# Kernel optimization log

Hardware: AMD Instinct MI355X
Metric: run time of the kernel (lower is better)

Reference implementation:

```python
import jax, jax.numpy as jnp
import numpy as np

EPS = 1e-5
GROUPS = 16
OUT_CH = 128
GC = OUT_CH // GROUPS  # group_channels = 8
SPAN = 128


def _bn(x, gamma, beta, axes):
    # BatchNorm in training mode: biased batch statistics over `axes`.
    m = jnp.mean(x, axis=axes, keepdims=True)
    v = jnp.var(x, axis=axes, keepdims=True)
    shape = [1] * x.ndim
    shape[1] = x.shape[1]
    g = gamma.reshape(shape)
    b = beta.reshape(shape)
    return (x - m) * jax.lax.rsqrt(v + EPS) * g + b


def setup_inputs() -> dict:
    key = jax.random.key(0)
    ks = jax.random.split(key, 3)
    x = jax.random.normal(ks[0], (2, 128, 64, 128), dtype=jnp.float32)
    W_qkv = jax.random.normal(ks[1], (2 * OUT_CH, 128), dtype=jnp.float32) * (1.0 / np.sqrt(128))
    rel_emb = jax.random.normal(ks[2], (2 * GC, 2 * SPAN - 1), dtype=jnp.float32)
    return {
        "x": x,
        "W_qkv": W_qkv,
        "gamma_qkv": jnp.ones((2 * OUT_CH,), jnp.float32),
        "beta_qkv": jnp.zeros((2 * OUT_CH,), jnp.float32),
        "rel_emb": rel_emb,
        "gamma_sim": jnp.ones((3 * GROUPS,), jnp.float32),
        "beta_sim": jnp.zeros((3 * GROUPS,), jnp.float32),
        "gamma_out": jnp.ones((2 * OUT_CH,), jnp.float32),
        "beta_out": jnp.zeros((2 * OUT_CH,), jnp.float32),
    }


def reference(x, W_qkv, gamma_qkv, beta_qkv, rel_emb, gamma_sim, beta_sim, gamma_out, beta_out):
    # dim == 1: attend over the width axis. x: [B, C, H, W], W == SPAN.
    B, C, H, W = x.shape
    xr = jnp.transpose(x, (0, 2, 1, 3)).reshape(B * H, C, W)  # [BH, C, W]

    # 1x1 Conv1d + BN1d -> query/key/value
    qkv = jnp.einsum('oc,bcl->bol', W_qkv, xr)  # [BH, 2*OUT, W]
    qkv = _bn(qkv, gamma_qkv, beta_qkv, axes=(0, 2))
    qkv = qkv.reshape(B * H, GROUPS, 2 * GC, W)
    q = qkv[:, :, : GC // 2]            # [BH, g, gc/2, W]
    k = qkv[:, :, GC // 2: GC]          # [BH, g, gc/2, W]
    v = qkv[:, :, GC:]                  # [BH, g, gc,   W]

    # relative position embeddings gathered into [2*gc, span, span]
    idx = jnp.arange(SPAN)[:, None] - jnp.arange(SPAN)[None, :] + SPAN - 1
    emb = rel_emb[:, idx]               # [2*gc, span, span]
    q_emb = emb[: GC // 2]
    k_emb = emb[GC // 2: GC]
    v_emb = emb[GC:]

    qe = jnp.einsum('bgci,cij->bgij', q, q_emb)   # [BH, g, W, W]
    ke = jnp.einsum('bgci,cij->bgij', k, k_emb)   # [BH, g, W, W]
    # faithful to original: contracts the first spatial axis of qe/ke
    qk = jnp.einsum('bgci,bgcj->bgij', qe, ke)    # [BH, g, W, W]

    sim = jnp.concatenate([qk, qe, ke], axis=1)   # [BH, 3g, W, W]
    sim = _bn(sim, gamma_sim, beta_sim, axes=(0, 2, 3))
    sim = sim.reshape(B * H, 3, GROUPS, W, W).sum(axis=1)  # [BH, g, W, W]
    sim = jax.nn.softmax(sim, axis=3)

    am = jnp.einsum('bgij,bgcj->bgci', sim, v)      # [BH, g, gc, W]
    ame = jnp.einsum('bgij,cij->bgci', sim, v_emb)  # [BH, g, gc, W]

    out = jnp.concatenate([am, ame], axis=-1).reshape(B * H, 2 * OUT_CH, W)
    out = _bn(out, gamma_out, beta_out, axes=(0, 2))
    out = out.reshape(B, H, OUT_CH, 2, W).sum(axis=-2)  # [B, H, OUT, W]
    return jnp.transpose(out, (0, 2, 1, 3))             # [B, OUT, H, W]
```

## Files before the change

kernel.cpp:

```cpp
#include <hip/hip_runtime.h>

#define EPS 1e-5f
typedef unsigned short u16;
typedef unsigned int u32;

typedef __attribute__((ext_vector_type(8))) short bf16x8;
typedef __attribute__((ext_vector_type(4))) float f32x4;

__device__ __forceinline__ float bf2f(u16 h) {
    u32 u = ((u32)h) << 16;
    return __builtin_bit_cast(float, u);
}
__device__ __forceinline__ u16 f2bf(float f) {
    u32 u = __builtin_bit_cast(u32, f);
    u32 r = (u + 0x7fffu + ((u >> 16) & 1u)) >> 16;
    return (u16)r;
}
__device__ __forceinline__ u32 pack2(float a, float b) {
    return (u32)f2bf(a) | ((u32)f2bf(b) << 16);
}

__global__ __launch_bounds__(256) void k1_gemm_qkv(
    const float* __restrict__ x, const float* __restrict__ Wq,
    float* __restrict__ qkv, float* __restrict__ stats)
{
    __shared__ float Wt[64 * 68];
    __shared__ float xt[64 * 128];
    const int tid = threadIdx.x;
    const int ot = blockIdx.x;
    const int n  = blockIdx.y;
    const int b = n >> 6, h = n & 63;
    const int to = tid >> 5, tl = tid & 31;
    const int o0 = to * 8, l0 = tl * 4;

    float acc[8][4];
#pragma unroll
    for (int r = 0; r < 8; ++r) { acc[r][0]=0.f; acc[r][1]=0.f; acc[r][2]=0.f; acc[r][3]=0.f; }

    for (int cb = 0; cb < 128; cb += 64) {
        __syncthreads();
#pragma unroll
        for (int k = 0; k < 4; ++k) {
            int f = tid + k * 256;
            int oo = f >> 4, c4 = f & 15;
            float4 v = *(const float4*)(Wq + (ot * 64 + oo) * 128 + cb + c4 * 4);
            *(float4*)(Wt + oo * 68 + c4 * 4) = v;
        }
#pragma unroll
        for (int k = 0; k < 8; ++k) {
            int f = tid + k * 256;
            int c = f >> 5, l4 = f & 31;
            float4 v = *(const float4*)(x + ((size_t)((b * 128 + cb + c) * 64 + h)) * 128 + l4 * 4);
            *(float4*)(xt + c * 128 + l4 * 4) = v;
        }
        __syncthreads();
#pragma unroll 4
        for (int c = 0; c < 64; ++c) {
            float4 xv = *(const float4*)(xt + c * 128 + l0);
#pragma unroll
            for (int r = 0; r < 8; ++r) {
                float w = Wt[(o0 + r) * 68 + c];
                acc[r][0] += w * xv.x; acc[r][1] += w * xv.y;
                acc[r][2] += w * xv.z; acc[r][3] += w * xv.w;
            }
        }
    }

#pragma unroll
    for (int r = 0; r < 8; ++r) {
        int o = ot * 64 + o0 + r;
        *(float4*)(qkv + ((size_t)n * 256 + o) * 128 + l0) =
            make_float4(acc[r][0], acc[r][1], acc[r][2], acc[r][3]);
        float s  = acc[r][0] + acc[r][1] + acc[r][2] + acc[r][3];
        float sq = acc[r][0]*acc[r][0] + acc[r][1]*acc[r][1] + acc[r][2]*acc[r][2] + acc[r][3]*acc[r][3];
#pragma unroll
        for (int m = 1; m < 32; m <<= 1) {
            s  += __shfl_xor(s, m);
            sq += __shfl_xor(sq, m);
        }
        if (tl == 0) {
            atomicAdd(&stats[o], s);
            atomicAdd(&stats[256 + o], sq);
        }
    }
}

__global__ void k3_coef_qkv(const float* __restrict__ stats,
                            const float* __restrict__ gamma, const float* __restrict__ beta,
                            float* __restrict__ coef)
{
    int o = threadIdx.x;
    const float cnt = 16384.f;
    float mean = stats[o] / cnt;
    float var  = stats[256 + o] / cnt - mean * mean;
    float a = gamma[o] * rsqrtf(var + EPS);
    coef[o] = a;
    coef[256 + o] = beta[o] - a * mean;
}

__global__ __launch_bounds__(512, 4) void k4_pass1(
    const float* __restrict__ qkv, const float* __restrict__ rel,
    const float* __restrict__ cq, u16* __restrict__ qk,
    float* __restrict__ stats)
{
    __shared__ u16 QEb[128 * 136];
    __shared__ u16 KEb[128 * 136];
    __shared__ float red[8 * 6];
    const int tid = threadIdx.x;
    const int n = blockIdx.x >> 4, g = blockIdx.x & 15;

    const int pt = tid & 31, pi = tid >> 5;
    const int t0 = pt * 4, i0 = pi * 8;
    const int d0 = t0 - i0 + 120;

    float qes = 0.f, qesq = 0.f, kes = 0.f, kesq = 0.f;

#pragma unroll
    for (int mat = 0; mat < 2; ++mat) {
        float qv[4][4];
#pragma unroll
        for (int c = 0; c < 4; ++c) {
            int o = g * 16 + mat * 4 + c;
            float a = cq[o], bb = cq[256 + o];
            float4 x0 = *(const float4*)(qkv + ((size_t)n * 256 + o) * 128 + t0);
            qv[c][0] = fmaf(a, x0.x, bb); qv[c][1] = fmaf(a, x0.y, bb);
            qv[c][2] = fmaf(a, x0.z, bb); qv[c][3] = fmaf(a, x0.w, bb);
        }
        float rr[4][12];
#pragma unroll
        for (int c = 0; c < 4; ++c) {
            const float* p = rel + (mat * 4 + c) * 255 + d0;
#pragma unroll
            for (int j = 0; j < 3; ++j) {
                float4 v = *(const float4*)(p + j * 4);
                rr[c][j*4+0] = v.x; rr[c][j*4+1] = v.y;
                rr[c][j*4+2] = v.z; rr[c][j*4+3] = v.w;
            }
        }
        u16* MB = mat ? KEb : QEb;
        float s = 0.f, sq = 0.f;
#pragma unroll
        for (int ii = 0; ii < 8; ++ii) {
            float vv[4];
#pragma unroll
            for (int tt = 0; tt < 4; ++tt) {
                int dl = tt - ii + 7;
                float v = qv[0][tt] * rr[0][dl] + qv[1][tt] * rr[1][dl]
                        + qv[2][tt] * rr[2][dl] + qv[3][tt] * rr[3][dl];
                vv[tt] = v;
                s += v; sq = fmaf(v, v, sq);
            }
            *(uint2*)(MB + (i0 + ii) * 136 + t0) =
                make_uint2(pack2(vv[0], vv[1]), pack2(vv[2], vv[3]));
        }
        if (mat == 0) { qes = s; qesq = sq; } else { kes = s; kesq = sq; }
    }
    __syncthreads();

    const int lane = tid & 63, wv = tid >> 6;
    const int fm = lane & 15, fq = lane >> 4;

    f32x4 acc[8];
#pragma unroll
    for (int tj = 0; tj < 8; ++tj) acc[tj] = (f32x4){0.f, 0.f, 0.f, 0.f};

#pragma unroll
    for (int kb = 0; kb < 4; ++kb) {
        const int ko = kb * 32 + fq * 8;
        bf16x8 a0 = *(const bf16x8*)(QEb + (wv * 16 + fm) * 136 + ko);
#pragma unroll
        for (int tj = 0; tj < 8; ++tj) {
            bf16x8 bfr = *(const bf16x8*)(KEb + (tj * 16 + fm) * 136 + ko);
            acc[tj] = __builtin_amdgcn_mfma_f32_16x16x32_bf16(a0, bfr, acc[tj], 0, 0, 0);
        }
    }

    float qks = 0.f, qksq = 0.f;
#pragma unroll
    for (int tj = 0; tj < 8; ++tj) {
#pragma unroll
        for (int r = 0; r < 4; ++r) {
            float v = acc[tj][r];
            qks += v; qksq = fmaf(v, v, qksq);
            QEb[(wv * 16 + fq * 4 + r) * 136 + tj * 16 + fm] = f2bf(v);
        }
    }

#pragma unroll
    for (int m = 1; m < 64; m <<= 1) {
        qes += __shfl_xor(qes, m);  qesq += __shfl_xor(qesq, m);
        kes += __shfl_xor(kes, m);  kesq += __shfl_xor(kesq, m);
        qks += __shfl_xor(qks, m);  qksq += __shfl_xor(qksq, m);
    }
    if (lane == 0) {
        red[wv * 6 + 0] = qes; red[wv * 6 + 1] = qesq;
        red[wv * 6 + 2] = kes; red[wv * 6 + 3] = kesq;
        red[wv * 6 + 4] = qks; red[wv * 6 + 5] = qksq;
    }
    __syncthreads();

    u16* qkg = qk + (size_t)(n * 16 + g) * 16384;
#pragma unroll
    for (int k = 0; k < 4; ++k) {
        int f = tid + k * 512;
        int row = f >> 4, c8 = f & 15;
        uint4 v = *(const uint4*)(QEb + row * 136 + c8 * 8);
        *(uint4*)(qkg + row * 128 + c8 * 8) = v;
    }

    if (tid < 6) {
        float tot = 0.f;
#pragma unroll
        for (int w = 0; w < 8; ++w) tot += red[w * 6 + tid];
        int off = (tid & 1) ? 560 : 512;
        int ch = (tid < 2) ? (16 + g) : (tid < 4) ? (32 + g) : g;
        atomicAdd(&stats[off + ch], tot);
    }
}

__global__ void k5_coef_sim(const float* __restrict__ stats,
                            const float* __restrict__ gamma, const float* __restrict__ beta,
                            float* __restrict__ coef)
{
    int ch = threadIdx.x;
    if (ch < 48) {
        const float cnt = 2097152.f;
        float mean = stats[512 + ch] / cnt;
        float var  = stats[560 + ch] / cnt - mean * mean;
        float a = gamma[ch] * rsqrtf(var + EPS);
        coef[ch] = a;
        coef[48 + ch] = beta[ch] - a * mean;
    }
}

__global__ __launch_bounds__(256, 4) void k6_pass2(
    const float* __restrict__ qkv, const float* __restrict__ rel,
    const float* __restrict__ cq, const float* __restrict__ cs,
    const u16* __restrict__ qk,
    float* __restrict__ outraw, float* __restrict__ ostats)
{
    __shared__ float relT[255 * 20];
    __shared__ float qv_s[2048];
    __shared__ float ot_s[16 * 132];
    const int tid = threadIdx.x;
    const int n = blockIdx.x >> 4, g = blockIdx.x & 15;

#pragma unroll
    for (int k = 0; k < 16; ++k) {
        int f = tid + k * 256;
        int d = f >> 4, c = f & 15;
        if (d < 255) relT[d * 20 + c] = rel[c * 255 + d];
    }
#pragma unroll
    for (int k = 0; k < 8; ++k) {
        int f = tid + k * 256;
        int row = f >> 7, t = f & 127;
        int o = g * 16 + row;
        qv_s[f] = cq[o] * qkv[((size_t)n * 256 + o) * 128 + t] + cq[256 + o];
    }
    __syncthreads();

    const float aqk = cs[g], aqe = cs[16 + g], ake = cs[32 + g];
    const float bsum = cs[48 + g] + cs[64 + g] + cs[80 + g];
    const int lane = tid & 63, wv = tid >> 6;
    const int r = lane >> 4, q = lane & 15;

    float vreg[8][8];
#pragma unroll
    for (int jj = 0; jj < 8; ++jj) {
        int j = q + 16 * jj;
#pragma unroll
        for (int c = 0; c < 8; ++c) vreg[jj][c] = qv_s[1024 + c * 128 + j];
    }
    const u16* qkg = qk + (size_t)(n * 16 + g) * 16384;

    for (int it = 0; it < 8; ++it) {
        int i = wv * 32 + it * 4 + r;
        float q0 = qv_s[i], q1 = qv_s[128 + i], q2 = qv_s[256 + i], q3 = qv_s[384 + i];
        float k0 = qv_s[512 + i], k1 = qv_s[640 + i], k2 = qv_s[768 + i], k3 = qv_s[896 + i];
        const u16* qkrow = qkg + i * 128;
        float s[8]; float mx = -3.0e38f;
#pragma unroll
        for (int jj = 0; jj < 8; ++jj) {
            int j = q + 16 * jj;
            int d = i - j + 127;
            float4 rq = *(const float4*)(relT + d * 20);
            float4 rk = *(const float4*)(relT + d * 20 + 4);
            float qe = q0 * rq.x + q1 * rq.y + q2 * rq.z + q3 * rq.w;
            float ke = k0 * rk.x + k1 * rk.y + k2 * rk.z + k3 * rk.w;
            float qkf = bf2f(qkrow[j]);
            float sv = aqk * qkf + aqe * qe + ake * ke + bsum;
            s[jj] = sv; mx = fmaxf(mx, sv);
        }
#pragma unroll
        for (int m = 1; m < 16; m <<= 1) mx = fmaxf(mx, __shfl_xor(mx, m));
        float es = 0.f; float e[8];
#pragma unroll
        for (int jj = 0; jj < 8; ++jj) { e[jj] = __expf(s[jj] - mx); es += e[jj]; }
#pragma unroll
        for (int m = 1; m < 16; m <<= 1) es += __shfl_xor(es, m);

        float am[8], ame[8];
#pragma unroll
        for (int c = 0; c < 8; ++c) { am[c] = 0.f; ame[c] = 0.f; }
#pragma unroll
        for (int jj = 0; jj < 8; ++jj) {
            int d = i - (q + 16 * jj) + 127;
            float4 r0 = *(const float4*)(relT + d * 20 + 8);
            float4 r1 = *(const float4*)(relT + d * 20 + 12);
            float ej = e[jj];
#pragma unroll
            for (int c = 0; c < 8; ++c) am[c] += ej * vreg[jj][c];
            ame[0] += ej * r0.x; ame[1] += ej * r0.y; ame[2] += ej * r0.z; ame[3] += ej * r0.w;
            ame[4] += ej * r1.x; ame[5] += ej * r1.y; ame[6] += ej * r1.z; ame[7] += ej * r1.w;
        }
#pragma unroll
        for (int m = 1; m < 16; m <<= 1) {
#pragma unroll
            for (int c = 0; c < 8; ++c) {
                am[c]  += __shfl_xor(am[c], m);
                ame[c] += __shfl_xor(ame[c], m);
            }
        }
        float inv = 1.f / es;
        float sel = 0.f;
#pragma unroll
        for (int c = 0; c < 8; ++c) {
            sel = (q == c)     ? am[c]  : sel;
            sel = (q == c + 8) ? ame[c] : sel;
        }
        int ch16 = (q < 8) ? (2 * q) : (2 * (q - 8) + 1);
        ot_s[ch16 * 132 + i] = sel * inv;
    }
    __syncthreads();

#pragma unroll
    for (int k = 0; k < 8; ++k) {
        int f = tid + k * 256;
        int ch16 = f >> 7, i = f & 127;
        float v = ot_s[ch16 * 132 + i];
        outraw[((size_t)n * 256 + g * 16 + ch16) * 128 + i] = v;
        float sv = v, sq = v * v;
#pragma unroll
        for (int m = 1; m < 64; m <<= 1) { sv += __shfl_xor(sv, m); sq += __shfl_xor(sq, m); }
        if (lane == 0) {
            atomicAdd(&ostats[g * 16 + ch16], sv);
            atomicAdd(&ostats[256 + g * 16 + ch16], sq);
        }
    }
}

__global__ void k7_coef_out(const float* __restrict__ stats,
                            const float* __restrict__ gamma, const float* __restrict__ beta,
                            float* __restrict__ coef)
{
    int o = threadIdx.x;
    const float cnt = 16384.f;
    float mean = stats[608 + o] / cnt;
    float var  = stats[864 + o] / cnt - mean * mean;
    float a = gamma[o] * rsqrtf(var + EPS);
    coef[o] = a;
    coef[256 + o] = beta[o] - a * mean;
}

__global__ __launch_bounds__(256) void k8_final(
    const float* __restrict__ outraw, const float* __restrict__ co,
    float* __restrict__ out)
{
    int idx = blockIdx.x * 256 + threadIdx.x;
    int w  = idx & 127;
    int h  = (idx >> 7) & 63;
    int oc = (idx >> 13) & 127;
    int b  = idx >> 20;
    int n  = b * 64 + h;
    int o0 = oc * 2;
    float x0 = outraw[((size_t)n * 256 + o0) * 128 + w];
    float x1 = outraw[((size_t)n * 256 + o0 + 1) * 128 + w];
    out[idx] = (co[o0] * x0 + co[256 + o0]) + (co[o0 + 1] * x1 + co[256 + o0 + 1]);
}

extern "C" void kernel_launch(void* const* d_in, const int* in_sizes, int n_in,
                              void* d_out, int out_size, void* d_ws, size_t ws_size,
                              hipStream_t stream)
{
    const float* x   = (const float*)d_in[0];
    const float* Wq  = (const float*)d_in[1];
    const float* gq  = (const float*)d_in[2];
    const float* bq  = (const float*)d_in[3];
    const float* rel = (const float*)d_in[4];
    const float* gs  = (const float*)d_in[5];
    const float* bs  = (const float*)d_in[6];
    const float* go  = (const float*)d_in[7];
    const float* bo  = (const float*)d_in[8];

    float* ws     = (float*)d_ws;
    float* qkv    = ws;
    float* outraw = ws + 4194304;
    u16*   qk     = (u16*)(ws + 8388608);
    float* stats  = ws + 25165824;
    float* cq     = stats + 1120;
    float* cs     = stats + 1632;
    float* co     = stats + 1728;

    (void)hipMemsetAsync(stats, 0, 1120 * sizeof(float), stream);

    k1_gemm_qkv<<<dim3(4, 128), 256, 0, stream>>>(x, Wq, qkv, stats);
    k3_coef_qkv<<<1, 256, 0, stream>>>(stats, gq, bq, cq);
    k4_pass1<<<2048, 512, 0, stream>>>(qkv, rel, cq, qk, stats);
    k5_coef_sim<<<1, 64, 0, stream>>>(stats, gs, bs, cs);
    k6_pass2<<<2048, 256, 0, stream>>>(qkv, rel, cq, cs, qk, outraw, stats + 608);
    k7_coef_out<<<1, 256, 0, stream>>>(stats, go, bo, co);
    k8_final<<<8192, 256, 0, stream>>>(outraw, co, (float*)d_out);
}
```

Measured before the change: 361.5 us.

## Rewrite attention pass as one-thread-per-row online softmax with bf16 LDS tables

```diff
diff --git a/kernel.cpp b/kernel.cpp
--- a/kernel.cpp
+++ b/kernel.cpp
@@ -233,119 +233,113 @@
     }
 }
 
-__global__ __launch_bounds__(256, 4) void k6_pass2(
+__global__ __launch_bounds__(128, 4) void k6_pass2(
     const float* __restrict__ qkv, const float* __restrict__ rel,
     const float* __restrict__ cq, const float* __restrict__ cs,
     const u16* __restrict__ qk,
     float* __restrict__ outraw, float* __restrict__ ostats)
 {
-    __shared__ float relT[255 * 20];
-    __shared__ float qv_s[2048];
-    __shared__ float ot_s[16 * 132];
+    __shared__ u16 relb[256 * 24];
+    __shared__ u16 vb[128 * 8];
+    __shared__ float qn_s[8 * 128];
     const int tid = threadIdx.x;
     const int n = blockIdx.x >> 4, g = blockIdx.x & 15;
 
 #pragma unroll
-    for (int k = 0; k < 16; ++k) {
-        int f = tid + k * 256;
-        int d = f >> 4, c = f & 15;
-        if (d < 255) relT[d * 20 + c] = rel[c * 255 + d];
+    for (int k = 0; k < 32; ++k) {
+        int f = tid + k * 128;
+        int c = f >> 8, d = f & 255;
+        if (d < 255) relb[d * 24 + c] = f2bf(rel[c * 255 + d]);
     }
 #pragma unroll
     for (int k = 0; k < 8; ++k) {
-        int f = tid + k * 256;
-        int row = f >> 7, t = f & 127;
-        int o = g * 16 + row;
-        qv_s[f] = cq[o] * qkv[((size_t)n * 256 + o) * 128 + t] + cq[256 + o];
+        int f = tid + k * 128;
+        int c = f >> 7, t = f & 127;
+        int o = g * 16 + c;
+        qn_s[f] = fmaf(cq[o], qkv[((size_t)n * 256 + o) * 128 + t], cq[256 + o]);
+    }
+#pragma unroll
+    for (int k = 0; k < 8; ++k) {
+        int f = tid + k * 128;
+        int c = f >> 7, j = f & 127;
+        int o = g * 16 + 8 + c;
+        float v = fmaf(cq[o], qkv[((size_t)n * 256 + o) * 128 + j], cq[256 + o]);
+        vb[j * 8 + c] = f2bf(v);
     }
     __syncthreads();
 
     const float aqk = cs[g], aqe = cs[16 + g], ake = cs[32 + g];
     const float bsum = cs[48 + g] + cs[64 + g] + cs[80 + g];
-    const int lane = tid & 63, wv = tid >> 6;
-    const int r = lane >> 4, q = lane & 15;
-
-    float vreg[8][8];
-#pragma unroll
-    for (int jj = 0; jj < 8; ++jj) {
-        int j = q + 16 * jj;
-#pragma unroll
-        for (int c = 0; c < 8; ++c) vreg[jj][c] = qv_s[1024 + c * 128 + j];
-    }
-    const u16* qkg = qk + (size_t)(n * 16 + g) * 16384;
-
-    for (int it = 0; it < 8; ++it) {
-        int i = wv * 32 + it * 4 + r;
-        float q0 = qv_s[i], q1 = qv_s[128 + i], q2 = qv_s[256 + i], q3 = qv_s[384 + i];
-        float k0 = qv_s[512 + i], k1 = qv_s[640 + i], k2 = qv_s[768 + i], k3 = qv_s[896 + i];
-        const u16* qkrow = qkg + i * 128;
-        float s[8]; float mx = -3.0e38f;
-#pragma unroll
-        for (int jj = 0; jj < 8; ++jj) {
-            int j = q + 16 * jj;
-            int d = i - j + 127;
-            float4 rq = *(const float4*)(relT + d * 20);
-            float4 rk = *(const float4*)(relT + d * 20 + 4);
-            float qe = q0 * rq.x + q1 * rq.y + q2 * rq.z + q3 * rq.w;
-            float ke = k0 * rk.x + k1 * rk.y + k2 * rk.z + k3 * rk.w;
-            float qkf = bf2f(qkrow[j]);
-            float sv = aqk * qkf + aqe * qe + ake * ke + bsum;
-            s[jj] = sv; mx = fmaxf(mx, sv);
-        }
-#pragma unroll
-        for (int m = 1; m < 16; m <<= 1) mx = fmaxf(mx, __shfl_xor(mx, m));
-        float es = 0.f; float e[8];
-#pragma unroll
-        for (int jj = 0; jj < 8; ++jj) { e[jj] = __expf(s[jj] - mx); es += e[jj]; }
-#pragma unroll
-        for (int m = 1; m < 16; m <<= 1) es += __shfl_xor(es, m);
-
-        float am[8], ame[8];
-#pragma unroll
-        for (int c = 0; c < 8; ++c) { am[c] = 0.f; ame[c] = 0.f; }
-#pragma unroll
-        for (int jj = 0; jj < 8; ++jj) {
-            int d = i - (q + 16 * jj) + 127;
-            float4 r0 = *(const float4*)(relT + d * 20 + 8);
-            float4 r1 = *(const float4*)(relT + d * 20 + 12);
-            float ej = e[jj];
-#pragma unroll
-            for (int c = 0; c < 8; ++c) am[c] += ej * vreg[jj][c];
-            ame[0] += ej * r0.x; ame[1] += ej * r0.y; ame[2] += ej * r0.z; ame[3] += ej * r0.w;
-            ame[4] += ej * r1.x; ame[5] += ej * r1.y; ame[6] += ej * r1.z; ame[7] += ej * r1.w;
-        }
-#pragma unroll
-        for (int m = 1; m < 16; m <<= 1) {
+    const int i = tid;
+
+    float q0 = qn_s[i],       q1 = qn_s[128 + i], q2 = qn_s[256 + i], q3 = qn_s[384 + i];
+    float k0 = qn_s[512 + i], k1 = qn_s[640 + i], k2 = qn_s[768 + i], k3 = qn_s[896 + i];
+
+    const u16* qkrow = qk + (size_t)(n * 16 + g) * 16384 + i * 128;
+
+    float m = -3.0e38f, l = 0.f;
+    float am[8], ame[8];
+#pragma unroll
+    for (int c = 0; c < 8; ++c) { am[c] = 0.f; ame[c] = 0.f; }
+
+#pragma unroll
+    for (int jc = 0; jc < 8; ++jc) {
+        union { uint4 v[2]; u16 h[16]; } qh;
+        qh.v[0] = *(const uint4*)(qkrow + jc * 16);
+        qh.v[1] = *(const uint4*)(qkrow + jc * 16 + 8);
+
+        const int dbase = i + 127 - jc * 16;
+        float s[16]; float mc = -3.0e38f;
+#pragma unroll
+        for (int jl = 0; jl < 16; ++jl) {
+            int d = dbase - jl;
+            bf16x8 rb = *(const bf16x8*)(relb + d * 24);
+            float qe = q0 * bf2f((u16)rb[0]) + q1 * bf2f((u16)rb[1])
+                     + q2 * bf2f((u16)rb[2]) + q3 * bf2f((u16)rb[3]);
+            float ke = k0 * bf2f((u16)rb[4]) + k1 * bf2f((u16)rb[5])
+                     + k2 * bf2f((u16)rb[6]) + k3 * bf2f((u16)rb[7]);
+            float sv = aqk * bf2f(qh.h[jl]) + aqe * qe + ake * ke + bsum;
+            s[jl] = sv; mc = fmaxf(mc, sv);
+        }
+        float mn = fmaxf(m, mc);
+        float sc = __expf(m - mn);
+        l *= sc;
+#pragma unroll
+        for (int c = 0; c < 8; ++c) { am[c] *= sc; ame[c] *= sc; }
+        m = mn;
+#pragma unroll
+        for (int jl = 0; jl < 16; ++jl) {
+            float e = __expf(s[jl] - m);
+            l += e;
+            int j = jc * 16 + jl;
+            bf16x8 vv = *(const bf16x8*)(vb + j * 8);
+            bf16x8 rv = *(const bf16x8*)(relb + (dbase - jl) * 24 + 8);
 #pragma unroll
             for (int c = 0; c < 8; ++c) {
-                am[c]  += __shfl_xor(am[c], m);
-                ame[c] += __shfl_xor(ame[c], m);
+                am[c]  = fmaf(e, bf2f((u16)vv[c]), am[c]);
+                ame[c] = fmaf(e, bf2f((u16)rv[c]), ame[c]);
             }
         }
-        float inv = 1.f / es;
-        float sel = 0.f;
-#pragma unroll
-        for (int c = 0; c < 8; ++c) {
-            sel = (q == c)     ? am[c]  : sel;
-            sel = (q == c + 8) ? ame[c] : sel;
-        }
-        int ch16 = (q < 8) ? (2 * q) : (2 * (q - 8) + 1);
-        ot_s[ch16 * 132 + i] = sel * inv;
-    }
-    __syncthreads();
-
-#pragma unroll
-    for (int k = 0; k < 8; ++k) {
-        int f = tid + k * 256;
-        int ch16 = f >> 7, i = f & 127;
-        float v = ot_s[ch16 * 132 + i];
-        outraw[((size_t)n * 256 + g * 16 + ch16) * 128 + i] = v;
-        float sv = v, sq = v * v;
-#pragma unroll
-        for (int m = 1; m < 64; m <<= 1) { sv += __shfl_xor(sv, m); sq += __shfl_xor(sq, m); }
+    }
+
+    float inv = 1.f / l;
+    float o16[16];
+#pragma unroll
+    for (int c = 0; c < 8; ++c) { o16[2 * c] = am[c] * inv; o16[2 * c + 1] = ame[c] * inv; }
+
+    float* orow = outraw + ((size_t)n * 256 + g * 16) * 128 + i;
+#pragma unroll
+    for (int c16 = 0; c16 < 16; ++c16) orow[c16 * 128] = o16[c16];
+
+    const int lane = tid & 63;
+#pragma unroll
+    for (int c16 = 0; c16 < 16; ++c16) {
+        float sv = o16[c16], sq = o16[c16] * o16[c16];
+#pragma unroll
+        for (int mm = 1; mm < 64; mm <<= 1) { sv += __shfl_xor(sv, mm); sq += __shfl_xor(sq, mm); }
         if (lane == 0) {
-            atomicAdd(&ostats[g * 16 + ch16], sv);
-            atomicAdd(&ostats[256 + g * 16 + ch16], sq);
+            atomicAdd(&ostats[g * 16 + c16], sv);
+            atomicAdd(&ostats[256 + g * 16 + c16], sq);
         }
     }
 }
@@ -408,7 +402,7 @@
     k3_coef_qkv<<<1, 256, 0, stream>>>(stats, gq, bq, cq);
     k4_pass1<<<2048, 512, 0, stream>>>(qkv, rel, cq, qk, stats);
     k5_coef_sim<<<1, 64, 0, stream>>>(stats, gs, bs, cs);
-    k6_pass2<<<2048, 256, 0, stream>>>(qkv, rel, cq, cs, qk, outraw, stats + 608);
+    k6_pass2<<<2048, 128, 0, stream>>>(qkv, rel, cq, cs, qk, outraw, stats + 608);
     k7_coef_out<<<1, 256, 0, stream>>>(stats, go, bo, co);
     k8_final<<<8192, 256, 0, stream>>>(outraw, co, (float*)d_out);
 }
```

New measurement: 345.9 us. 1.04x faster.
